# Performance work log

Measured on AMD Instinct MI355X. Metric: run time of the kernel, lower is better.

## Reference

```python
import jax, jax.numpy as jnp
import numpy as np

N = 50000
IN_CH = 128
HEADS = 4
OUT_CH = 16
HID = HEADS * OUT_CH  # 64
E = 800000
B_EXP = 2.0
EPS = 1e-06
LN_EPS = 1e-05

def _l2norm(v, axis):
    n = jnp.sqrt(jnp.sum(v * v, axis=axis, keepdims=True))
    return v / jnp.maximum(n, 1e-12)  # matches F.normalize eps

def setup_inputs() -> dict:
    key = jax.random.key(0)
    k1, k2, k3, k4 = jax.random.split(key, 4)
    x = jax.random.normal(k1, (N, IN_CH), dtype=jnp.float32)
    edge_index = jax.random.randint(k2, (2, E), 0, N, dtype=jnp.int64)
    # lin: xavier_uniform over [HID, IN_CH]
    bound = float(np.sqrt(6.0 / (HID + IN_CH)))
    lin_w = jax.random.uniform(k3, (HID, IN_CH), dtype=jnp.float32, minval=-bound, maxval=bound)
    bcos_w = jax.random.normal(k4, (HID, HID), dtype=jnp.float32) * (1.0 / np.sqrt(HID))
    ln_gamma = jnp.ones((HID,), dtype=jnp.float32)
    ln_beta = jnp.zeros((HID,), dtype=jnp.float32)
    return {"x": x, "edge_index": edge_index, "lin_w": lin_w,
            "bcos_w": bcos_w, "ln_gamma": ln_gamma, "ln_beta": ln_beta}

def reference(x, edge_index, lin_w, bcos_w, ln_gamma, ln_beta):
    row, col = edge_index[0], edge_index[1]
    h = (x @ lin_w.T).reshape(N, HEADS, OUT_CH)          # [N,H,D]
    h_norm = _l2norm(h, axis=2)
    # per-edge cosine between source (col) and target (row) node features
    cos = jnp.sum(h_norm[col] * h_norm[row], axis=2)     # [E,H]
    cos = jnp.clip(cos, EPS, 1.0)
    scale = cos ** (B_EXP - 1.0)                         # [E,H]
    messages = h[col] * scale[:, :, None]                # [E,H,D]
    # scatter-add messages to target nodes
    out = jax.ops.segment_sum(messages.reshape(E, HID), row, num_segments=N)  # [N,HID]
    # BcosLinearNoBias
    lin = out @ bcos_w.T
    o_n = _l2norm(out, axis=1)
    w_n = _l2norm(bcos_w, axis=1)
    cos2 = jnp.clip(o_n @ w_n.T, EPS, 1.0)
    out_bcos = lin * cos2 ** (B_EXP - 1.0)
    # LayerNorm
    mu = jnp.mean(out_bcos, axis=-1, keepdims=True)
    var = jnp.mean((out_bcos - mu) ** 2, axis=-1, keepdims=True)
    out_norm = (out_bcos - mu) / jnp.sqrt(var + LN_EPS) * ln_gamma + ln_beta
    # dropout is identity in eval mode
    return out_norm
```

## Files before the change

kernel.cpp:

```cpp
#include <hip/hip_runtime.h>
#include <math.h>

#define N_NODES 50000
#define IN_CH   128
#define HEADS   4
#define HID     64
#define NEDGE   800000
#define EPS     1e-6f
#define LN_EPS  1e-5f
#define PAD     48
#define MTILES  (N_NODES / 16)
#define SEGS    100
#define SEG     8000
#define NG      12500

typedef __attribute__((ext_vector_type(8))) _Float16 f16x8;
typedef __attribute__((ext_vector_type(4))) float    f32x4;

#define DPP_ADD_F(p, ctrl) \
    p += __int_as_float(__builtin_amdgcn_update_dpp(0, __float_as_int(p), ctrl, 0xF, 0xF, true))
#define REDUCE16_DPP(p) { DPP_ADD_F(p,0xB1); DPP_ADD_F(p,0x4E); \
                          DPP_ADD_F(p,0x141); DPP_ADD_F(p,0x140); }
#define REDUCE4_DPP(p)  { DPP_ADD_F(p,0xB1); DPP_ADD_F(p,0x4E); }
#define REDUCE64(p) { REDUCE16_DPP(p); p += __shfl_xor(p,16); p += __shfl_xor(p,32); }

__global__ __launch_bounds__(512) void cnt_kernel(const int* __restrict__ ei,
                                                  unsigned* __restrict__ cnt,
                                                  unsigned char* __restrict__ lrank) {
    __shared__ unsigned lc[NG];
    for (int i = threadIdx.x; i < NG; i += 512) lc[i] = 0u;
    __syncthreads();
    int base = blockIdx.x * SEG;
#pragma unroll 1
    for (int it = 0; it < SEG / 512 + 1; ++it) {
        int el = it * 512 + threadIdx.x;
        if (el < SEG) {
            int e = base + el;
            int n = ei[e];
            unsigned sh  = 8u * (n & 3);
            unsigned old = atomicAdd(&lc[n >> 2], 1u << sh);
            lrank[e] = (unsigned char)((old >> sh) & 0xFFu);
        }
    }
    __syncthreads();
    for (int i = threadIdx.x; i < NG; i += 512)
        cnt[blockIdx.x * NG + i] = lc[i];
}

__global__ __launch_bounds__(256) void prefix_kernel(unsigned* __restrict__ cnt,
                                                     unsigned* __restrict__ deg4) {
    int g = blockIdx.x * 256 + threadIdx.x;
    if (g >= NG) return;
    unsigned run = 0u;
#pragma unroll 1
    for (int s = 0; s < SEGS; s += 4) {
        unsigned c0 = cnt[(s + 0) * NG + g];
        unsigned c1 = cnt[(s + 1) * NG + g];
        unsigned c2 = cnt[(s + 2) * NG + g];
        unsigned c3 = cnt[(s + 3) * NG + g];
        cnt[(s + 0) * NG + g] = run; run += c0;
        cnt[(s + 1) * NG + g] = run; run += c1;
        cnt[(s + 2) * NG + g] = run; run += c2;
        cnt[(s + 3) * NG + g] = run; run += c3;
    }
    deg4[g] = run;
}

__device__ __forceinline__ void gemm_mtile(int mt, const float* __restrict__ x,
                                           const float* __restrict__ lin_w,
                                           float* __restrict__ h,
                                           float* __restrict__ inv_hn, int lane) {
    int node0 = mt * 16;
    int mrow  = lane & 15;
    int kg    = lane >> 4;
    const float4* xp = (const float4*)x;
    const float4* w4 = (const float4*)lin_w;

    f16x8 A[4];
#pragma unroll
    for (int s = 0; s < 4; ++s) {
        float4 u0 = xp[(node0 + mrow) * 32 + s * 8 + kg * 2];
        float4 u1 = xp[(node0 + mrow) * 32 + s * 8 + kg * 2 + 1];
        f16x8 a;
        a[0] = (_Float16)u0.x; a[1] = (_Float16)u0.y;
        a[2] = (_Float16)u0.z; a[3] = (_Float16)u0.w;
        a[4] = (_Float16)u1.x; a[5] = (_Float16)u1.y;
        a[6] = (_Float16)u1.z; a[7] = (_Float16)u1.w;
        A[s] = a;
    }
#pragma unroll
    for (int nt = 0; nt < 4; ++nt) {
        f32x4 C = {0.f, 0.f, 0.f, 0.f};
#pragma unroll
        for (int s = 0; s < 4; ++s) {
            int wrow = nt * 16 + mrow;
            float4 u0 = w4[wrow * 32 + s * 8 + kg * 2];
            float4 u1 = w4[wrow * 32 + s * 8 + kg * 2 + 1];
            f16x8 b;
            b[0] = (_Float16)u0.x; b[1] = (_Float16)u0.y;
            b[2] = (_Float16)u0.z; b[3] = (_Float16)u0.w;
            b[4] = (_Float16)u1.x; b[5] = (_Float16)u1.y;
            b[6] = (_Float16)u1.z; b[7] = (_Float16)u1.w;
            C = __builtin_amdgcn_mfma_f32_16x16x32_f16(A[s], b, C, 0, 0, 0);
        }
        float ss0 = C[0] * C[0], ss1 = C[1] * C[1];
        float ss2 = C[2] * C[2], ss3 = C[3] * C[3];
#pragma unroll
        for (int rr = 0; rr < 4; ++rr)
            h[(node0 + 4 * kg + rr) * HID + nt * 16 + mrow] = C[rr];
        REDUCE16_DPP(ss0); REDUCE16_DPP(ss1);
        REDUCE16_DPP(ss2); REDUCE16_DPP(ss3);
        if (mrow == 0) {
            inv_hn[(node0 + 4 * kg + 0) * HEADS + nt] = 1.0f / fmaxf(sqrtf(ss0), 1e-12f);
            inv_hn[(node0 + 4 * kg + 1) * HEADS + nt] = 1.0f / fmaxf(sqrtf(ss1), 1e-12f);
            inv_hn[(node0 + 4 * kg + 2) * HEADS + nt] = 1.0f / fmaxf(sqrtf(ss2), 1e-12f);
            inv_hn[(node0 + 4 * kg + 3) * HEADS + nt] = 1.0f / fmaxf(sqrtf(ss3), 1e-12f);
        }
    }
}

__global__ __launch_bounds__(256, 4) void fill_h_kernel(const float* __restrict__ x,
                                                        const float* __restrict__ lin_w,
                                                        float* __restrict__ h,
                                                        float* __restrict__ inv_hn,
                                                        const int* __restrict__ ei,
                                                        const unsigned* __restrict__ sbase,
                                                        const unsigned char* __restrict__ lrank,
                                                        int* __restrict__ csr_col) {
    int lane = threadIdx.x & 63;
    int wave = threadIdx.x >> 6;

    int t = blockIdx.x * 256 + threadIdx.x;
    bool have_e = (t < NEDGE / 4);
    int4 r, c; unsigned lr4 = 0;
    int sb0 = 0, sb1 = 0, sb2 = 0, sb3 = 0;
    if (have_e) {
        r   = ((const int4*)ei)[t];
        c   = ((const int4*)(ei + NEDGE))[t];
        lr4 = ((const unsigned*)lrank)[t];
        int s = t / (SEG / 4);
        sb0 = (sbase[s * NG + (r.x >> 2)] >> (8 * (r.x & 3))) & 0xFF;
        sb1 = (sbase[s * NG + (r.y >> 2)] >> (8 * (r.y & 3))) & 0xFF;
        sb2 = (sbase[s * NG + (r.z >> 2)] >> (8 * (r.z & 3))) & 0xFF;
        sb3 = (sbase[s * NG + (r.w >> 2)] >> (8 * (r.w & 3))) & 0xFF;
    }

    int mt = blockIdx.x * 4 + wave;
    if (mt < MTILES) gemm_mtile(mt, x, lin_w, h, inv_hn, lane);

    if (have_e) {
        int sl0 = sb0 + ((lr4 >> 0)  & 0xFF);
        int sl1 = sb1 + ((lr4 >> 8)  & 0xFF);
        int sl2 = sb2 + ((lr4 >> 16) & 0xFF);
        int sl3 = sb3 + ((lr4 >> 24) & 0xFF);
        if (sl0 < PAD) __builtin_nontemporal_store(c.x, &csr_col[r.x * PAD + sl0]);
        if (sl1 < PAD) __builtin_nontemporal_store(c.y, &csr_col[r.y * PAD + sl1]);
        if (sl2 < PAD) __builtin_nontemporal_store(c.z, &csr_col[r.z * PAD + sl2]);
        if (sl3 < PAD) __builtin_nontemporal_store(c.w, &csr_col[r.w * PAD + sl3]);
    }
}

__global__ __launch_bounds__(256) void fill_kernel(const int* __restrict__ ei,
                                                   const unsigned* __restrict__ sbase,
                                                   const unsigned char* __restrict__ lrank,
                                                   int* __restrict__ csr_col) {
    int t = blockIdx.x * 256 + threadIdx.x;
    if (t >= NEDGE / 4) return;
    int s = t / (SEG / 4);
    int4 r = ((const int4*)ei)[t];
    int4 c = ((const int4*)(ei + NEDGE))[t];
    unsigned lr4 = ((const unsigned*)lrank)[t];
    int sl0 = ((sbase[s * NG + (r.x >> 2)] >> (8 * (r.x & 3))) & 0xFF) + ((lr4 >> 0)  & 0xFF);
    int sl1 = ((sbase[s * NG + (r.y >> 2)] >> (8 * (r.y & 3))) & 0xFF) + ((lr4 >> 8)  & 0xFF);
    int sl2 = ((sbase[s * NG + (r.z >> 2)] >> (8 * (r.z & 3))) & 0xFF) + ((lr4 >> 16) & 0xFF);
    int sl3 = ((sbase[s * NG + (r.w >> 2)] >> (8 * (r.w & 3))) & 0xFF) + ((lr4 >> 24) & 0xFF);
    if (sl0 < PAD) __builtin_nontemporal_store(c.x, &csr_col[r.x * PAD + sl0]);
    if (sl1 < PAD) __builtin_nontemporal_store(c.y, &csr_col[r.y * PAD + sl1]);
    if (sl2 < PAD) __builtin_nontemporal_store(c.z, &csr_col[r.z * PAD + sl2]);
    if (sl3 < PAD) __builtin_nontemporal_store(c.w, &csr_col[r.w * PAD + sl3]);
}

__global__ __launch_bounds__(256, 4) void h_kernel(const float* __restrict__ x,
                                                   const float* __restrict__ lin_w,
                                                   float* __restrict__ h,
                                                   float* __restrict__ inv_hn) {
    int mt = blockIdx.x * 4 + (threadIdx.x >> 6);
    if (mt < MTILES) gemm_mtile(mt, x, lin_w, h, inv_hn, threadIdx.x & 63);
}

__global__ __launch_bounds__(256, 4) void gather_final(const unsigned char* __restrict__ deg8,
                                                       const int* __restrict__ csr_col,
                                                       const float* __restrict__ h,
                                                       const float* __restrict__ inv_hn,
                                                       const float* __restrict__ bcos_w,
                                                       const float* __restrict__ gamma,
                                                       const float* __restrict__ beta,
                                                       float* __restrict__ y) {
    __shared__ float4 wt4[16][65];
    __shared__ float rowbuf[4][HID];
    __shared__ float ivw[HID], gm[HID], bt[HID];

    for (int i = threadIdx.x; i < HID * (HID / 4); i += 256) {
        int j = i >> 4, k4 = i & 15;
        wt4[k4][j] = ((const float4*)bcos_w)[i];
    }
    if (threadIdx.x < HID) {
        gm[threadIdx.x] = gamma[threadIdx.x];
        bt[threadIdx.x] = beta[threadIdx.x];
    }
    __syncthreads();
    if (threadIdx.x < HID) {
        float ss = 0.f;
#pragma unroll
        for (int k4 = 0; k4 < 16; ++k4) {
            float4 q = wt4[k4][threadIdx.x];
            ss += q.x * q.x + q.y * q.y + q.z * q.z + q.w * q.w;
        }
        ivw[threadIdx.x] = 1.0f / fmaxf(sqrtf(ss), 1e-12f);
    }
    __syncthreads();

    int grp    = threadIdx.x >> 6;
    int lane   = threadIdx.x & 63;
    int e_slot = lane >> 4;
    int ch4    = lane & 15;
    int hd     = ch4 >> 2;

    const float4* h4 = (const float4*)h;

    for (int g = blockIdx.x; g < N_NODES / 4; g += gridDim.x) {
        int node = g * 4 + grp;
        float4 hq  = h4[node * 16 + ch4];
        float  ihr = inv_hn[node * HEADS + hd];
        float4 hrs4 = make_float4(hq.x * ihr, hq.y * ihr, hq.z * ihr, hq.w * ihr);
        int dg    = __builtin_amdgcn_readfirstlane(min((int)deg8[node], PAD));
        int start = node * PAD;

        float4 acc = make_float4(0.f, 0.f, 0.f, 0.f);
#pragma unroll 1
        for (int bb = 0; bb < dg; bb += 16) {
            int   cc[4];
            float4 hh[4];
            float ii[4];
#pragma unroll
            for (int s = 0; s < 4; ++s) {
                int e = bb + s * 4 + e_slot;
                int ix = (e < dg) ? e : dg - 1;
                cc[s] = csr_col[start + ix];
            }
#pragma unroll
            for (int s = 0; s < 4; ++s) hh[s] = h4[cc[s] * 16 + ch4];
#pragma unroll
            for (int s = 0; s < 4; ++s) ii[s] = inv_hn[cc[s] * HEADS + hd];
#pragma unroll
            for (int s = 0; s < 4; ++s) {
                float p = hh[s].x * hrs4.x + hh[s].y * hrs4.y
                        + hh[s].z * hrs4.z + hh[s].w * hrs4.w;
                REDUCE4_DPP(p);
                float sc = fminf(fmaxf(p * ii[s], EPS), 1.0f);
                int e = bb + s * 4 + e_slot;
                sc = (e < dg) ? sc : 0.0f;
                acc.x = fmaf(hh[s].x, sc, acc.x);
                acc.y = fmaf(hh[s].y, sc, acc.y);
                acc.z = fmaf(hh[s].z, sc, acc.z);
                acc.w = fmaf(hh[s].w, sc, acc.w);
            }
        }
        acc.x += __shfl_xor(acc.x, 16); acc.x += __shfl_xor(acc.x, 32);
        acc.y += __shfl_xor(acc.y, 16); acc.y += __shfl_xor(acc.y, 32);
        acc.z += __shfl_xor(acc.z, 16); acc.z += __shfl_xor(acc.z, 32);
        acc.w += __shfl_xor(acc.w, 16); acc.w += __shfl_xor(acc.w, 32);

        if (lane < 16) ((float4*)rowbuf[grp])[ch4] = acc;
        float o = rowbuf[grp][lane];

        float ss = o * o;
        REDUCE64(ss);
        float inv_no = 1.0f / fmaxf(sqrtf(ss), 1e-12f);

        const float4* rb4 = (const float4*)rowbuf[grp];
        float lin = 0.f;
#pragma unroll
        for (int k4 = 0; k4 < 16; ++k4) {
            float4 a  = rb4[k4];
            float4 wv = wt4[k4][lane];
            lin += a.x * wv.x + a.y * wv.y + a.z * wv.z + a.w * wv.w;
        }

        float c2v = lin * inv_no * ivw[lane];
        c2v = fminf(fmaxf(c2v, EPS), 1.0f);
        float ob = lin * c2v;

        float mu = ob;
        REDUCE64(mu);
        mu *= (1.0f / 64.0f);
        float d = ob - mu;
        float var = d * d;
        REDUCE64(var);
        var *= (1.0f / 64.0f);
        float r = rsqrtf(var + LN_EPS);
        y[node * HID + lane] = d * r * gm[lane] + bt[lane];
    }
}

extern "C" void kernel_launch(void* const* d_in, const int* in_sizes, int n_in,
                              void* d_out, int out_size, void* d_ws, size_t ws_size,
                              hipStream_t stream) {
    const float* x      = (const float*)d_in[0];
    const int*   ei     = (const int*)d_in[1];
    const float* lin_w  = (const float*)d_in[2];
    const float* bcos_w = (const float*)d_in[3];
    const float* gamma  = (const float*)d_in[4];
    const float* beta   = (const float*)d_in[5];
    float*       y      = (float*)d_out;

    const size_t CNT_B   = (size_t)SEGS * NG * 4;
    const size_t LRANK_B = NEDGE;
    const size_t H_B     = (size_t)N_NODES * HID * 4;
    const size_t INV_B   = (size_t)N_NODES * HEADS * 4;
    const size_t DEG_B   = NG * 4;
    const size_t CSR_B   = (size_t)N_NODES * PAD * 4;

    if (ws_size >= CNT_B + LRANK_B + H_B + INV_B + DEG_B + CSR_B) {
        char* p = (char*)d_ws;
        unsigned* cnt        = (unsigned*)p;            p += CNT_B;
        unsigned char* lrank = (unsigned char*)p;       p += LRANK_B;
        float* h             = (float*)p;               p += H_B;
        float* inv_hn        = (float*)p;               p += INV_B;
        unsigned* deg4       = (unsigned*)p;            p += DEG_B;
        int* csr_col         = (int*)p;

        cnt_kernel<<<SEGS, 512, 0, stream>>>(ei, cnt, lrank);
        prefix_kernel<<<(NG + 255) / 256, 256, 0, stream>>>(cnt, deg4);
        fill_h_kernel<<<(MTILES + 3) / 4, 256, 0, stream>>>(x, lin_w, h, inv_hn,
                                                            ei, cnt, lrank, csr_col);
        gather_final<<<2048, 256, 0, stream>>>((const unsigned char*)deg4, csr_col,
                                               h, inv_hn, bcos_w, gamma, beta, y);
    } else {
        float* h             = (float*)d_ws;
        unsigned* cnt        = (unsigned*)d_ws;
        unsigned char* lrank = (unsigned char*)d_ws + CNT_B;
        float* inv_hn        = h + (size_t)N_NODES * HID;
        unsigned* deg4       = (unsigned*)(inv_hn + (size_t)N_NODES * HEADS);
        int* csr_col         = (int*)(deg4 + NG);

        cnt_kernel<<<SEGS, 512, 0, stream>>>(ei, cnt, lrank);
        prefix_kernel<<<(NG + 255) / 256, 256, 0, stream>>>(cnt, deg4);
        fill_kernel<<<(NEDGE / 4 + 255) / 256, 256, 0, stream>>>(ei, cnt, lrank, csr_col);
        h_kernel<<<(MTILES + 3) / 4, 256, 0, stream>>>(x, lin_w, h, inv_hn);
        gather_final<<<2048, 256, 0, stream>>>((const unsigned char*)deg4, csr_col,
                                               h, inv_hn, bcos_w, gamma, beta, y);
    }
}
```

Measured before the change: 120.0 us.

## Move node GEMM into counting kernel and double edge segments

The per-node linear projection and norm computation now runs inside the edge-counting kernel instead of the CSR fill kernel. The edge list is split into 200 segments of 4000 edges instead of 100 of 8000, which doubles the number of counting blocks and the size of the count/prefix arrays. The aim is to use the otherwise idle compute in the small-grid, atomic-bound counting pass to hide the GEMM, and to give that pass more parallelism. The cost is a prefix scan over twice as many segments, and the fallback workspace layout changes as well.

Result: slower. 131.7 us (+9.8%).

```diff
diff --git a/kernel.cpp b/kernel.cpp
--- a/kernel.cpp
+++ b/kernel.cpp
@@ -10,8 +10,6 @@
 #define LN_EPS  1e-5f
 #define PAD     48
 #define MTILES  (N_NODES / 16)
-#define SEGS    100
-#define SEG     8000
 #define NG      12500
 
 typedef __attribute__((ext_vector_type(8))) _Float16 f16x8;
@@ -23,48 +21,6 @@
                           DPP_ADD_F(p,0x141); DPP_ADD_F(p,0x140); }
 #define REDUCE4_DPP(p)  { DPP_ADD_F(p,0xB1); DPP_ADD_F(p,0x4E); }
 #define REDUCE64(p) { REDUCE16_DPP(p); p += __shfl_xor(p,16); p += __shfl_xor(p,32); }
-
-__global__ __launch_bounds__(512) void cnt_kernel(const int* __restrict__ ei,
-                                                  unsigned* __restrict__ cnt,
-                                                  unsigned char* __restrict__ lrank) {
-    __shared__ unsigned lc[NG];
-    for (int i = threadIdx.x; i < NG; i += 512) lc[i] = 0u;
-    __syncthreads();
-    int base = blockIdx.x * SEG;
-#pragma unroll 1
-    for (int it = 0; it < SEG / 512 + 1; ++it) {
-        int el = it * 512 + threadIdx.x;
-        if (el < SEG) {
-            int e = base + el;
-            int n = ei[e];
-            unsigned sh  = 8u * (n & 3);
-            unsigned old = atomicAdd(&lc[n >> 2], 1u << sh);
-            lrank[e] = (unsigned char)((old >> sh) & 0xFFu);
-        }
-    }
-    __syncthreads();
-    for (int i = threadIdx.x; i < NG; i += 512)
-        cnt[blockIdx.x * NG + i] = lc[i];
-}
-
-__global__ __launch_bounds__(256) void prefix_kernel(unsigned* __restrict__ cnt,
-                                                     unsigned* __restrict__ deg4) {
-    int g = blockIdx.x * 256 + threadIdx.x;
-    if (g >= NG) return;
-    unsigned run = 0u;
-#pragma unroll 1
-    for (int s = 0; s < SEGS; s += 4) {
-        unsigned c0 = cnt[(s + 0) * NG + g];
-        unsigned c1 = cnt[(s + 1) * NG + g];
-        unsigned c2 = cnt[(s + 2) * NG + g];
-        unsigned c3 = cnt[(s + 3) * NG + g];
-        cnt[(s + 0) * NG + g] = run; run += c0;
-        cnt[(s + 1) * NG + g] = run; run += c1;
-        cnt[(s + 2) * NG + g] = run; run += c2;
-        cnt[(s + 3) * NG + g] = run; run += c3;
-    }
-    deg4[g] = run;
-}
 
 __device__ __forceinline__ void gemm_mtile(int mt, const float* __restrict__ x,
                                            const float* __restrict__ lin_w,
@@ -119,17 +75,75 @@
     }
 }
 
-__global__ __launch_bounds__(256, 4) void fill_h_kernel(const float* __restrict__ x,
-                                                        const float* __restrict__ lin_w,
-                                                        float* __restrict__ h,
-                                                        float* __restrict__ inv_hn,
-                                                        const int* __restrict__ ei,
-                                                        const unsigned* __restrict__ sbase,
-                                                        const unsigned char* __restrict__ lrank,
-                                                        int* __restrict__ csr_col) {
-    int lane = threadIdx.x & 63;
-    int wave = threadIdx.x >> 6;
-
+template<int SEGSN, int SEGN, bool FUSE_GEMM>
+__global__ __launch_bounds__(512) void cnt_kernel(const int* __restrict__ ei,
+                                                  unsigned* __restrict__ cnt,
+                                                  unsigned char* __restrict__ lrank,
+                                                  const float* __restrict__ x,
+                                                  const float* __restrict__ lin_w,
+                                                  float* __restrict__ h,
+                                                  float* __restrict__ inv_hn) {
+    __shared__ unsigned lc[NG];
+    for (int i = threadIdx.x; i < NG; i += 512) lc[i] = 0u;
+    __syncthreads();
+    int base = blockIdx.x * SEGN;
+#pragma unroll 1
+    for (int it = 0; it < SEGN / 512 + 1; ++it) {
+        int el = it * 512 + threadIdx.x;
+        if (el < SEGN) {
+            int e = base + el;
+            int n = ei[e];
+            unsigned sh  = 8u * (n & 3);
+            unsigned old = atomicAdd(&lc[n >> 2], 1u << sh);
+            lrank[e] = (unsigned char)((old >> sh) & 0xFFu);
+        }
+    }
+
+    if (FUSE_GEMM) {
+        int wave = threadIdx.x >> 6;
+        int lane = threadIdx.x & 63;
+        const int TPW = (MTILES + SEGSN * 8 - 1) / (SEGSN * 8);
+#pragma unroll
+        for (int j = 0; j < TPW; ++j) {
+            int mt = blockIdx.x * (8 * TPW) + j * 8 + wave;
+            if (mt < MTILES) gemm_mtile(mt, x, lin_w, h, inv_hn, lane);
+        }
+    }
+
+    __syncthreads();
+    for (int i = threadIdx.x; i < NG; i += 512)
+        cnt[blockIdx.x * NG + i] = lc[i];
+}
+
+template<int SEGSN>
+__global__ __launch_bounds__(256) void prefix_kernel(unsigned* __restrict__ cnt,
+                                                     unsigned* __restrict__ deg4) {
+    int g = blockIdx.x * 256 + threadIdx.x;
+    if (g >= NG) return;
+    unsigned run = 0u;
+#pragma unroll 1
+    for (int s = 0; s < SEGSN; s += 4) {
+        unsigned c0 = cnt[(s + 0) * NG + g];
+        unsigned c1 = cnt[(s + 1) * NG + g];
+        unsigned c2 = cnt[(s + 2) * NG + g];
+        unsigned c3 = cnt[(s + 3) * NG + g];
+        cnt[(s + 0) * NG + g] = run; run += c0;
+        cnt[(s + 1) * NG + g] = run; run += c1;
+        cnt[(s + 2) * NG + g] = run; run += c2;
+        cnt[(s + 3) * NG + g] = run; run += c3;
+    }
+    deg4[g] = run;
+}
+
+template<int SEGN, bool WITH_GEMM>
+__global__ __launch_bounds__(256, 4) void fill_kernel(const int* __restrict__ ei,
+                                                      const unsigned* __restrict__ sbase,
+                                                      const unsigned char* __restrict__ lrank,
+                                                      int* __restrict__ csr_col,
+                                                      const float* __restrict__ x,
+                                                      const float* __restrict__ lin_w,
+                                                      float* __restrict__ h,
+                                                      float* __restrict__ inv_hn) {
     int t = blockIdx.x * 256 + threadIdx.x;
     bool have_e = (t < NEDGE / 4);
     int4 r, c; unsigned lr4 = 0;
@@ -138,15 +152,17 @@
         r   = ((const int4*)ei)[t];
         c   = ((const int4*)(ei + NEDGE))[t];
         lr4 = ((const unsigned*)lrank)[t];
-        int s = t / (SEG / 4);
+        int s = t / (SEGN / 4);
         sb0 = (sbase[s * NG + (r.x >> 2)] >> (8 * (r.x & 3))) & 0xFF;
         sb1 = (sbase[s * NG + (r.y >> 2)] >> (8 * (r.y & 3))) & 0xFF;
         sb2 = (sbase[s * NG + (r.z >> 2)] >> (8 * (r.z & 3))) & 0xFF;
         sb3 = (sbase[s * NG + (r.w >> 2)] >> (8 * (r.w & 3))) & 0xFF;
     }
 
-    int mt = blockIdx.x * 4 + wave;
-    if (mt < MTILES) gemm_mtile(mt, x, lin_w, h, inv_hn, lane);
+    if (WITH_GEMM) {
+        int mt = blockIdx.x * 4 + (threadIdx.x >> 6);
+        if (mt < MTILES) gemm_mtile(mt, x, lin_w, h, inv_hn, threadIdx.x & 63);
+    }
 
     if (have_e) {
         int sl0 = sb0 + ((lr4 >> 0)  & 0xFF);
@@ -158,34 +174,6 @@
         if (sl2 < PAD) __builtin_nontemporal_store(c.z, &csr_col[r.z * PAD + sl2]);
         if (sl3 < PAD) __builtin_nontemporal_store(c.w, &csr_col[r.w * PAD + sl3]);
     }
-}
-
-__global__ __launch_bounds__(256) void fill_kernel(const int* __restrict__ ei,
-                                                   const unsigned* __restrict__ sbase,
-                                                   const unsigned char* __restrict__ lrank,
-                                                   int* __restrict__ csr_col) {
-    int t = blockIdx.x * 256 + threadIdx.x;
-    if (t >= NEDGE / 4) return;
-    int s = t / (SEG / 4);
-    int4 r = ((const int4*)ei)[t];
-    int4 c = ((const int4*)(ei + NEDGE))[t];
-    unsigned lr4 = ((const unsigned*)lrank)[t];
-    int sl0 = ((sbase[s * NG + (r.x >> 2)] >> (8 * (r.x & 3))) & 0xFF) + ((lr4 >> 0)  & 0xFF);
-    int sl1 = ((sbase[s * NG + (r.y >> 2)] >> (8 * (r.y & 3))) & 0xFF) + ((lr4 >> 8)  & 0xFF);
-    int sl2 = ((sbase[s * NG + (r.z >> 2)] >> (8 * (r.z & 3))) & 0xFF) + ((lr4 >> 16) & 0xFF);
-    int sl3 = ((sbase[s * NG + (r.w >> 2)] >> (8 * (r.w & 3))) & 0xFF) + ((lr4 >> 24) & 0xFF);
-    if (sl0 < PAD) __builtin_nontemporal_store(c.x, &csr_col[r.x * PAD + sl0]);
-    if (sl1 < PAD) __builtin_nontemporal_store(c.y, &csr_col[r.y * PAD + sl1]);
-    if (sl2 < PAD) __builtin_nontemporal_store(c.z, &csr_col[r.z * PAD + sl2]);
-    if (sl3 < PAD) __builtin_nontemporal_store(c.w, &csr_col[r.w * PAD + sl3]);
-}
-
-__global__ __launch_bounds__(256, 4) void h_kernel(const float* __restrict__ x,
-                                                   const float* __restrict__ lin_w,
-                                                   float* __restrict__ h,
-                                                   float* __restrict__ inv_hn) {
-    int mt = blockIdx.x * 4 + (threadIdx.x >> 6);
-    if (mt < MTILES) gemm_mtile(mt, x, lin_w, h, inv_hn, threadIdx.x & 63);
 }
 
 __global__ __launch_bounds__(256, 4) void gather_final(const unsigned char* __restrict__ deg8,
@@ -314,40 +302,44 @@
     const float* beta   = (const float*)d_in[5];
     float*       y      = (float*)d_out;
 
-    const size_t CNT_B   = (size_t)SEGS * NG * 4;
     const size_t LRANK_B = NEDGE;
     const size_t H_B     = (size_t)N_NODES * HID * 4;
     const size_t INV_B   = (size_t)N_NODES * HEADS * 4;
     const size_t DEG_B   = NG * 4;
     const size_t CSR_B   = (size_t)N_NODES * PAD * 4;
-
-    if (ws_size >= CNT_B + LRANK_B + H_B + INV_B + DEG_B + CSR_B) {
+    const size_t CNT200  = (size_t)200 * NG * 4;
+    const size_t CNT100  = (size_t)100 * NG * 4;
+
+    if (ws_size >= CNT200 + LRANK_B + H_B + INV_B + DEG_B + CSR_B) {
         char* p = (char*)d_ws;
-        unsigned* cnt        = (unsigned*)p;            p += CNT_B;
+        unsigned* cnt        = (unsigned*)p;            p += CNT200;
         unsigned char* lrank = (unsigned char*)p;       p += LRANK_B;
         float* h             = (float*)p;               p += H_B;
         float* inv_hn        = (float*)p;               p += INV_B;
         unsigned* deg4       = (unsigned*)p;            p += DEG_B;
         int* csr_col         = (int*)p;
 
-        cnt_kernel<<<SEGS, 512, 0, stream>>>(ei, cnt, lrank);
-        prefix_kernel<<<(NG + 255) / 256, 256, 0, stream>>>(cnt, deg4);
-        fill_h_kernel<<<(MTILES + 3) / 4, 256, 0, stream>>>(x, lin_w, h, inv_hn,
-                                                            ei, cnt, lrank, csr_col);
+        cnt_kernel<200, 4000, true><<<200, 512, 0, stream>>>(ei, cnt, lrank,
+                                                             x, lin_w, h, inv_hn);
+        prefix_kernel<200><<<(NG + 255) / 256, 256, 0, stream>>>(cnt, deg4);
+        fill_kernel<4000, false><<<(NEDGE / 4 + 255) / 256, 256, 0, stream>>>(
+            ei, cnt, lrank, csr_col, x, lin_w, h, inv_hn);
         gather_final<<<2048, 256, 0, stream>>>((const unsigned char*)deg4, csr_col,
                                                h, inv_hn, bcos_w, gamma, beta, y);
     } else {
-        float* h             = (float*)d_ws;
-        unsigned* cnt        = (unsigned*)d_ws;
-        unsigned char* lrank = (unsigned char*)d_ws + CNT_B;
-        float* inv_hn        = h + (size_t)N_NODES * HID;
-        unsigned* deg4       = (unsigned*)(inv_hn + (size_t)N_NODES * HEADS);
-        int* csr_col         = (int*)(deg4 + NG);
-
-        cnt_kernel<<<SEGS, 512, 0, stream>>>(ei, cnt, lrank);
-        prefix_kernel<<<(NG + 255) / 256, 256, 0, stream>>>(cnt, deg4);
-        fill_kernel<<<(NEDGE / 4 + 255) / 256, 256, 0, stream>>>(ei, cnt, lrank, csr_col);
-        h_kernel<<<(MTILES + 3) / 4, 256, 0, stream>>>(x, lin_w, h, inv_hn);
+        char* p = (char*)d_ws;
+        unsigned* cnt        = (unsigned*)p;            p += CNT100;
+        unsigned char* lrank = (unsigned char*)p;       p += LRANK_B;
+        float* h             = (float*)p;               p += H_B;
+        float* inv_hn        = (float*)p;               p += INV_B;
+        unsigned* deg4       = (unsigned*)p;            p += DEG_B;
+        int* csr_col         = (int*)p;
+
+        cnt_kernel<100, 8000, false><<<100, 512, 0, stream>>>(ei, cnt, lrank,
+                                                              x, lin_w, h, inv_hn);
+        prefix_kernel<100><<<(NG + 255) / 256, 256, 0, stream>>>(cnt, deg4);
+        fill_kernel<8000, true><<<(MTILES + 3) / 4, 256, 0, stream>>>(
+            ei, cnt, lrank, csr_col, x, lin_w, h, inv_hn);
         gather_final<<<2048, 256, 0, stream>>>((const unsigned char*)deg4, csr_col,
                                                h, inv_hn, bcos_w, gamma, beta, y);
     }
```
